# Optimization experiments

Hardware: AMD Instinct MI355X
Metric: run time of the kernel (lower is better)

## Reference

```python
import jax, jax.numpy as jnp
import numpy as np

NUM_CAPSULE = 32
DIM_CAPSULE = 16
ROUTINGS = 3
IN_CAPS = 144
IN_DIM = 8
EPS = 1e-7  # keras.backend.epsilon()


def setup_inputs() -> dict:
    key = jax.random.key(0)
    k1, k2 = jax.random.split(key)
    inputs = jax.random.normal(k1, (512, IN_CAPS, IN_DIM), dtype=jnp.float32)
    # glorot_uniform over shape [num_capsule, 144, dim_capsule, 8]
    fan_in, fan_out = IN_CAPS * IN_DIM, NUM_CAPSULE * DIM_CAPSULE
    limit = np.sqrt(6.0 / (fan_in + fan_out)).astype(np.float32)
    W = jax.random.uniform(k2, (NUM_CAPSULE, IN_CAPS, DIM_CAPSULE, IN_DIM),
                           minval=-limit, maxval=limit, dtype=jnp.float32)
    return {"inputs": inputs, "W": W}


def _squash(s):
    # s: [..., dim_capsule]
    n2 = jnp.sum(s * s, axis=-1, keepdims=True)
    return (n2 / (1.0 + n2)) * s / jnp.sqrt(n2 + EPS)


def reference(inputs, W):
    # inputs: [B, 144, 8]; W: [num_capsule, 144, dim_capsule, 8]
    # tile+einsum('abci,bcji->abcj') == broadcasted contraction over i
    inputs_hat = jnp.einsum('aci,bcji->abcj', inputs, W)  # [B, nc, 144, dc]
    b = jnp.zeros(inputs_hat.shape[:3], dtype=inputs_hat.dtype)  # [B, nc, 144]
    outputs = None
    for i in range(ROUTINGS):
        c = jax.nn.softmax(b, axis=1)                      # over num_capsule
        s = jnp.einsum('abc,abcd->abd', c, inputs_hat)     # [B, nc, dc]
        outputs = _squash(s)
        if i < ROUTINGS - 1:
            b = b + jnp.einsum('abd,abcd->abc', outputs, inputs_hat)
    return outputs
```

## Files before the change

kernel.cpp:

```cpp
#include <hip/hip_runtime.h>

#define NC 32
#define DC 16
#define INC 144
#define IND 8
#define NT 512
#define LG_S 152

#define HATL_OFF 0
#define HATH_OFF (NC * INC * IND + 8)
#define LG_OFF (HATH_OFF + NC * INC * IND)
#define OB_OFF (LG_OFF + NC * LG_S)
#define SMEM_HALVES (OB_OFF + NC * DC)
#define SMEM_BYTES (SMEM_HALVES * 2)

typedef _Float16 h2 __attribute__((ext_vector_type(2)));
typedef _Float16 h4v __attribute__((ext_vector_type(4)));
typedef _Float16 h8 __attribute__((ext_vector_type(8)));
typedef float f4 __attribute__((ext_vector_type(4)));

union H8 { h8 v; h2 p[4]; _Float16 e[8]; };
union WU { uint4 u; h8 v; h2 p[4]; };

#if __has_builtin(__builtin_amdgcn_fdot2)
__device__ __forceinline__ float fdot2(h2 a, h2 b, float c) {
    return __builtin_amdgcn_fdot2(a, b, c, false);
}
#else
__device__ __forceinline__ float fdot2(h2 a, h2 b, float c) {
    return c + (float)a[0] * (float)b[0] + (float)a[1] * (float)b[1];
}
#endif

__global__ void convw_kernel(const float* __restrict__ W, _Float16* __restrict__ Wh) {
    int i = blockIdx.x * 256 + threadIdx.x;
    int cg = i & 15, d = (i >> 4) & 15, bk = i >> 8;
    int k = bk % 9, b = bk / 9;
    const float* s = W + (((size_t)b * INC + cg + 16 * k) * DC + d) * IND;
    f4 v0 = *reinterpret_cast<const f4*>(s);
    f4 v1 = *reinterpret_cast<const f4*>(s + 4);
    H8 o;
    o.e[0] = (_Float16)v0[0]; o.e[1] = (_Float16)v0[1];
    o.e[2] = (_Float16)v0[2]; o.e[3] = (_Float16)v0[3];
    o.e[4] = (_Float16)v1[0]; o.e[5] = (_Float16)v1[1];
    o.e[6] = (_Float16)v1[2]; o.e[7] = (_Float16)v1[3];
    *reinterpret_cast<h8*>(Wh + (size_t)i * 8) = o.v;
}

#define R9(M)  M(0) M(1) M(2) M(3) M(4) M(5) M(6) M(7) M(8)
#define R16(M) M(0) M(1) M(2) M(3) M(4) M(5) M(6) M(7) M(8) M(9) M(10) M(11) M(12) M(13) M(14) M(15)

template <typename WT>
__global__ __launch_bounds__(NT)
__attribute__((amdgpu_waves_per_eu(2, 4)))
void caps_kernel(const float* __restrict__ xg, const WT* __restrict__ Wg,
                 float* __restrict__ out) {
    extern __shared__ __align__(16) _Float16 sm[];
    _Float16* lg = sm + LG_OFF;
    _Float16* o_buf = sm + OB_OFF;
    _Float16* x_h = lg;

    const int t = threadIdx.x;
    const int b = t >> 4;
    const int cg = t & 15;
    const int a = blockIdx.x;

    if (t < 288) {
        f4 v = reinterpret_cast<const f4*>(xg + (size_t)a * (INC * IND))[t];
        h4v hv;
        hv[0] = (_Float16)v[0]; hv[1] = (_Float16)v[1];
        hv[2] = (_Float16)v[2]; hv[3] = (_Float16)v[3];
        *reinterpret_cast<h4v*>(x_h + t * 4) = hv;
    }
    __syncthreads();

#define DECLS(D) float s##D;
    R16(DECLS)
#define ZEROS(D) s##D = 0.f;
    R16(ZEROS)

#define WADDR(K, DG) reinterpret_cast<const uint4*>( \
    reinterpret_cast<const char*>(Wg) + (size_t)(b * 9 + (K)) * 4096 + (DG) * 256 + cg * 16)

#define PREA(K) { wA0 = *WADDR(K,0); wA1 = *WADDR(K,1); wA2 = *WADDR(K,2); \
                  wA3 = *WADDR(K,3); wA4 = *WADDR(K,4); wA5 = *WADDR(K,5); \
                  wA6 = *WADDR(K,6); wA7 = *WADDR(K,7); }
#define PREB(K) { wB0 = *WADDR(K,8); wB1 = *WADDR(K,9); wB2 = *WADDR(K,10); \
                  wB3 = *WADDR(K,11); wB4 = *WADDR(K,12); wB5 = *WADDR(K,13); \
                  wB6 = *WADDR(K,14); wB7 = *WADDR(K,15); }

#define HD1R(WREG, T, E, SD) { \
    WU w; w.u = WREG; \
    float ac = fdot2(w.p[0], xv.p[0], 0.f); \
    ac = fdot2(w.p[1], xv.p[1], ac); \
    ac = fdot2(w.p[2], xv.p[2], ac); \
    ac = fdot2(w.p[3], xv.p[3], ac); \
    T.e[E] = (_Float16)ac; s##SD += ac; }

#define CMPA(T) HD1R(wA0,T,0,0) HD1R(wA1,T,1,1) HD1R(wA2,T,2,2) HD1R(wA3,T,3,3) \
                HD1R(wA4,T,4,4) HD1R(wA5,T,5,5) HD1R(wA6,T,6,6) HD1R(wA7,T,7,7)
#define CMPB(T) HD1R(wB0,T,0,8) HD1R(wB1,T,1,9) HD1R(wB2,T,2,10) HD1R(wB3,T,3,11) \
                HD1R(wB4,T,4,12) HD1R(wB5,T,5,13) HD1R(wB6,T,6,14) HD1R(wB7,T,7,15)

#define HPIPE(K, KN) { \
    const int c = cg + 16 * (K); \
    H8 xv; xv.v = *reinterpret_cast<const h8*>(x_h + c * IND); \
    H8 tL, tH; \
    CMPA(tL) \
    PREA(KN) \
    CMPB(tH) \
    PREB(KN) \
    *reinterpret_cast<h8*>(sm + HATL_OFF + (size_t)(b * INC + c) * 8) = tL.v; \
    *reinterpret_cast<h8*>(sm + HATH_OFF + (size_t)(b * INC + c) * 8) = tH.v; }

#define HD1F(T, E, DG) { \
    const float* wf = wfr + (DG) * IND; \
    f4 w0 = *reinterpret_cast<const f4*>(wf); \
    f4 w1 = *reinterpret_cast<const f4*>(wf + 4); \
    float ac = (float)xv.e[0] * w0[0]; \
    ac = fmaf((float)xv.e[1], w0[1], ac); \
    ac = fmaf((float)xv.e[2], w0[2], ac); \
    ac = fmaf((float)xv.e[3], w0[3], ac); \
    ac = fmaf((float)xv.e[4], w1[0], ac); \
    ac = fmaf((float)xv.e[5], w1[1], ac); \
    ac = fmaf((float)xv.e[6], w1[2], ac); \
    ac = fmaf((float)xv.e[7], w1[3], ac); \
    T.e[E] = (_Float16)ac; s##DG += ac; }

#define HSTEPF(K) { \
    const int c = cg + 16 * (K); \
    H8 xv; xv.v = *reinterpret_cast<const h8*>(x_h + c * IND); \
    const float* wfr = reinterpret_cast<const float*>(Wg) + \
                       (size_t)(b * INC + c) * (DC * IND); \
    H8 tL, tH; \
    HD1F(tL,0,0) HD1F(tL,1,1) HD1F(tL,2,2) HD1F(tL,3,3) \
    HD1F(tL,4,4) HD1F(tL,5,5) HD1F(tL,6,6) HD1F(tL,7,7) \
    HD1F(tH,0,8) HD1F(tH,1,9) HD1F(tH,2,10) HD1F(tH,3,11) \
    HD1F(tH,4,12) HD1F(tH,5,13) HD1F(tH,6,14) HD1F(tH,7,15) \
    *reinterpret_cast<h8*>(sm + HATL_OFF + (size_t)(b * INC + c) * 8) = tL.v; \
    *reinterpret_cast<h8*>(sm + HATH_OFF + (size_t)(b * INC + c) * 8) = tH.v; }

    if constexpr (sizeof(WT) == 2) {
        uint4 wA0, wA1, wA2, wA3, wA4, wA5, wA6, wA7;
        uint4 wB0, wB1, wB2, wB3, wB4, wB5, wB6, wB7;
        PREA(0) PREB(0)
        HPIPE(0, 1) HPIPE(1, 2) HPIPE(2, 3) HPIPE(3, 4) HPIPE(4, 5)
        HPIPE(5, 6) HPIPE(6, 7) HPIPE(7, 8) HPIPE(8, 8)
    } else {
        R9(HSTEPF)
    }
    __syncthreads();

    const bool c8 = (cg & 8) != 0, c4 = (cg & 4) != 0;
    const bool c2 = (cg & 2) != 0, c1 = (cg & 1) != 0;
#define HV(A, B, M, CB) { float snd_ = (CB) ? s##A : s##B; \
                          float kp_ = (CB) ? s##B : s##A; \
                          s##A = kp_ + __shfl_xor(snd_, M, 16); }
#define HALVE16 \
    HV(0,8,8,c8) HV(1,9,8,c8) HV(2,10,8,c8) HV(3,11,8,c8) \
    HV(4,12,8,c8) HV(5,13,8,c8) HV(6,14,8,c8) HV(7,15,8,c8) \
    HV(0,4,4,c4) HV(1,5,4,c4) HV(2,6,4,c4) HV(3,7,4,c4) \
    HV(0,2,2,c2) HV(1,3,2,c2) \
    HV(0,1,1,c1)

#define SQUASH1(RS, OVAL) \
    float r_ = s0 * (RS); \
    float n2_ = r_ * r_; \
    n2_ += __shfl_xor(n2_, 1, 16); n2_ += __shfl_xor(n2_, 2, 16); \
    n2_ += __shfl_xor(n2_, 4, 16); n2_ += __shfl_xor(n2_, 8, 16); \
    float OVAL = r_ * (n2_ / ((1.0f + n2_) * sqrtf(n2_ + 1e-7f)));

#define OBCAST(OVAL) \
    o_buf[b * DC + cg] = (_Float16)(OVAL); \
    __threadfence_block(); \
    oLv = *reinterpret_cast<const h8*>(o_buf + b * DC); \
    oHv = *reinterpret_cast<const h8*>(o_buf + b * DC + 8);

    h8 oLv, oHv;
    HALVE16
    {
        SQUASH1(1.0f / 32.0f, oval)
        OBCAST(oval)
    }

#define DECLG(K) float lgr##K = 0.f;
    R9(DECLG)

#define BSTEP(K) { \
    const int c = cg + 16 * (K); \
    H8 hl, hh; \
    hl.v = *reinterpret_cast<const h8*>(sm + HATL_OFF + (size_t)(b * INC + c) * 8); \
    hh.v = *reinterpret_cast<const h8*>(sm + HATH_OFF + (size_t)(b * INC + c) * 8); \
    H8 ol, oh; ol.v = oLv; oh.v = oHv; \
    float dt  = fdot2(hl.p[0], ol.p[0], 0.f); \
    float dt2 = fdot2(hl.p[1], ol.p[1], 0.f); \
    dt  = fdot2(hl.p[2], ol.p[2], dt); \
    dt2 = fdot2(hl.p[3], ol.p[3], dt2); \
    dt  = fdot2(hh.p[0], oh.p[0], dt); \
    dt2 = fdot2(hh.p[1], oh.p[1], dt2); \
    dt  = fdot2(hh.p[2], oh.p[2], dt); \
    dt2 = fdot2(hh.p[3], oh.p[3], dt2); \
    lgr##K += dt + dt2; \
    lg[b * LG_S + c] = (_Float16)lgr##K; }

#define SSTEP(K) { \
    const int c = cg + 16 * (K); \
    float cf = (float)lg[b * LG_S + c]; \
    H8 hl, hh; \
    hl.v = *reinterpret_cast<const h8*>(sm + HATL_OFF + (size_t)(b * INC + c) * 8); \
    hh.v = *reinterpret_cast<const h8*>(sm + HATH_OFF + (size_t)(b * INC + c) * 8); \
    s0  = fmaf(cf, (float)hl.e[0], s0);  s1  = fmaf(cf, (float)hl.e[1], s1); \
    s2  = fmaf(cf, (float)hl.e[2], s2);  s3  = fmaf(cf, (float)hl.e[3], s3); \
    s4  = fmaf(cf, (float)hl.e[4], s4);  s5  = fmaf(cf, (float)hl.e[5], s5); \
    s6  = fmaf(cf, (float)hl.e[6], s6);  s7  = fmaf(cf, (float)hl.e[7], s7); \
    s8  = fmaf(cf, (float)hh.e[0], s8);  s9  = fmaf(cf, (float)hh.e[1], s9); \
    s10 = fmaf(cf, (float)hh.e[2], s10); s11 = fmaf(cf, (float)hh.e[3], s11); \
    s12 = fmaf(cf, (float)hh.e[4], s12); s13 = fmaf(cf, (float)hh.e[5], s13); \
    s14 = fmaf(cf, (float)hh.e[6], s14); s15 = fmaf(cf, (float)hh.e[7], s15); }

    for (int it = 0; it < 2; ++it) {
        R9(BSTEP)
        __syncthreads();

        if (t < 2 * INC) {
            const int c = t >> 1;
            const int rb = (t & 1) * 16;
#define SMR(I) float v##I = (float)lg[(rb + I) * LG_S + c];
            R16(SMR)
            float m = fmaxf(v0, v1);
#define SMM(I) m = fmaxf(m, v##I);
            SMM(2) SMM(3) SMM(4) SMM(5) SMM(6) SMM(7) SMM(8) SMM(9)
            SMM(10) SMM(11) SMM(12) SMM(13) SMM(14) SMM(15)
            m = fmaxf(m, __shfl_xor(m, 1));
            float S = 0.f;
#define SME(I) v##I = __expf(v##I - m); S += v##I;
            R16(SME)
            S += __shfl_xor(S, 1);
            float inv = 1.0f / S;
#define SMW(I) lg[(rb + I) * LG_S + c] = (_Float16)(v##I * inv);
            R16(SMW)
        }
        __syncthreads();

        R16(ZEROS)
        R9(SSTEP)
        HALVE16

        if (it == 0) {
            SQUASH1(1.0f, oval)
            OBCAST(oval)
            __syncthreads();
        } else {
            SQUASH1(1.0f, oval)
            out[(size_t)a * (NC * DC) + t] = oval;
        }
    }
}

extern "C" void kernel_launch(void* const* d_in, const int* in_sizes, int n_in,
                              void* d_out, int out_size, void* d_ws, size_t ws_size,
                              hipStream_t stream) {
    const float* x = (const float*)d_in[0];
    const float* W = (const float*)d_in[1];
    float* out = (float*)d_out;

    const size_t WH_BYTES = (size_t)NC * INC * DC * IND * 2;

    if (ws_size >= WH_BYTES) {
        _Float16* Wh = (_Float16*)d_ws;
        hipLaunchKernelGGL(convw_kernel, dim3(288), dim3(256), 0, stream, W, Wh);
        hipFuncSetAttribute(reinterpret_cast<const void*>(&caps_kernel<_Float16>),
                            hipFuncAttributeMaxDynamicSharedMemorySize, SMEM_BYTES);
        hipLaunchKernelGGL(caps_kernel<_Float16>, dim3(512), dim3(NT), SMEM_BYTES,
                           stream, x, Wh, out);
    } else {
        hipFuncSetAttribute(reinterpret_cast<const void*>(&caps_kernel<float>),
                            hipFuncAttributeMaxDynamicSharedMemorySize, SMEM_BYTES);
        hipLaunchKernelGGL(caps_kernel<float>, dim3(512), dim3(NT), SMEM_BYTES,
                           stream, x, W, out);
    }
}
```

Measured before the change: 44.72 us.

## Split hat computation into separate kernel writing fp16 u_hat to global workspace

Adds a hat_kernel that caches one capsule's fp16 weights in LDS and computes inputs_hat for 16 batch rows per block, writing the results to global memory. A route_kernel then loads u_hat into LDS and runs routing only, with the first iteration's sum done by a plain reduction. The goal is to stop each routing block from streaming all weights out of global or L2 memory. In exchange it writes and rereads about 75 MB of u_hat through HBM and adds an extra launch. It needs a larger workspace, and the old fused path is kept as a fallback.

Measured after the change: 86.93 us. 94.4% more time.

```diff
diff --git a/kernel.cpp b/kernel.cpp
--- a/kernel.cpp
+++ b/kernel.cpp
@@ -13,6 +13,12 @@
 #define OB_OFF (LG_OFF + NC * LG_S)
 #define SMEM_HALVES (OB_OFF + NC * DC)
 #define SMEM_BYTES (SMEM_HALVES * 2)
+
+#define WH_BYTES ((size_t)NC * INC * DC * IND * 2)
+#define PLANE_HALVES ((size_t)512 * NC * INC * IND)
+#define PLANE_BYTES (PLANE_HALVES * 2)
+#define NEED_BYTES (WH_BYTES + 2 * PLANE_BYTES)
+#define HSM_BYTES 73728
 
 typedef _Float16 h2 __attribute__((ext_vector_type(2)));
 typedef _Float16 h4v __attribute__((ext_vector_type(4)));
@@ -47,30 +53,89 @@
     *reinterpret_cast<h8*>(Wh + (size_t)i * 8) = o.v;
 }
 
+#define R8(M)  M(0) M(1) M(2) M(3) M(4) M(5) M(6) M(7)
 #define R9(M)  M(0) M(1) M(2) M(3) M(4) M(5) M(6) M(7) M(8)
 #define R16(M) M(0) M(1) M(2) M(3) M(4) M(5) M(6) M(7) M(8) M(9) M(10) M(11) M(12) M(13) M(14) M(15)
 
-template <typename WT>
+__global__ __launch_bounds__(256)
+void hat_kernel(const float* __restrict__ xg, const _Float16* __restrict__ Wh,
+                _Float16* __restrict__ hatLg, _Float16* __restrict__ hatHg) {
+    extern __shared__ __align__(16) _Float16 hsm[];
+    _Float16* Wl = hsm;
+    _Float16* xl = hsm + 18432;
+
+    const int t = threadIdx.x;
+    const int b = blockIdx.x & 31;
+    const int ach = blockIdx.x >> 5;
+
+    {
+        const h8* src = reinterpret_cast<const h8*>(Wh + (size_t)b * 18432);
+        h8* dst = reinterpret_cast<h8*>(Wl);
+        #pragma unroll
+        for (int j = 0; j < 9; ++j) dst[t + 256 * j] = src[t + 256 * j];
+    }
+    {
+        const f4* src = reinterpret_cast<const f4*>(xg) + (size_t)ach * 4608;
+        #pragma unroll
+        for (int j = 0; j < 18; ++j) {
+            int i = t + 256 * j;
+            f4 v = src[i];
+            h4v hv;
+            hv[0] = (_Float16)v[0]; hv[1] = (_Float16)v[1];
+            hv[2] = (_Float16)v[2]; hv[3] = (_Float16)v[3];
+            *reinterpret_cast<h4v*>(xl + (size_t)i * 4) = hv;
+        }
+    }
+    __syncthreads();
+
+    const int al = t >> 4, cg = t & 15;
+    const size_t rowbase = (((size_t)(ach * 16 + al) * NC + b) * INC + cg * 9) * 8;
+
+#define WD1(T, E, D) { \
+    WU w; w.u = *reinterpret_cast<const uint4*>(Wl + ((kk * 16 + (D)) * 16 + cg) * 8); \
+    float ac = fdot2(w.p[0], xv.p[0], 0.f); \
+    ac = fdot2(w.p[1], xv.p[1], ac); \
+    ac = fdot2(w.p[2], xv.p[2], ac); \
+    ac = fdot2(w.p[3], xv.p[3], ac); \
+    T.e[E] = (_Float16)ac; }
+
+#define HK(K) { \
+    const int kk = (K); \
+    const int c = cg + 16 * kk; \
+    H8 xv; xv.v = *reinterpret_cast<const h8*>(xl + ((size_t)al * INC + c) * 8); \
+    H8 tL, tH; \
+    WD1(tL,0,0) WD1(tL,1,1) WD1(tL,2,2) WD1(tL,3,3) \
+    WD1(tL,4,4) WD1(tL,5,5) WD1(tL,6,6) WD1(tL,7,7) \
+    WD1(tH,0,8) WD1(tH,1,9) WD1(tH,2,10) WD1(tH,3,11) \
+    WD1(tH,4,12) WD1(tH,5,13) WD1(tH,6,14) WD1(tH,7,15) \
+    *reinterpret_cast<h8*>(hatLg + rowbase + (size_t)kk * 8) = tL.v; \
+    *reinterpret_cast<h8*>(hatHg + rowbase + (size_t)kk * 8) = tH.v; }
+
+    R9(HK)
+}
+
 __global__ __launch_bounds__(NT)
 __attribute__((amdgpu_waves_per_eu(2, 4)))
-void caps_kernel(const float* __restrict__ xg, const WT* __restrict__ Wg,
-                 float* __restrict__ out) {
+void route_kernel(const _Float16* __restrict__ hatLg, const _Float16* __restrict__ hatHg,
+                  float* __restrict__ out) {
     extern __shared__ __align__(16) _Float16 sm[];
     _Float16* lg = sm + LG_OFF;
     _Float16* o_buf = sm + OB_OFF;
-    _Float16* x_h = lg;
 
     const int t = threadIdx.x;
     const int b = t >> 4;
     const int cg = t & 15;
     const int a = blockIdx.x;
 
-    if (t < 288) {
-        f4 v = reinterpret_cast<const f4*>(xg + (size_t)a * (INC * IND))[t];
-        h4v hv;
-        hv[0] = (_Float16)v[0]; hv[1] = (_Float16)v[1];
-        hv[2] = (_Float16)v[2]; hv[3] = (_Float16)v[3];
-        *reinterpret_cast<h4v*>(x_h + t * 4) = hv;
+    {
+        const h8* srcL = reinterpret_cast<const h8*>(hatLg + (size_t)a * 36864);
+        const h8* srcH = reinterpret_cast<const h8*>(hatHg + (size_t)a * 36864);
+        #pragma unroll
+        for (int j = 0; j < 9; ++j) {
+            int i = t + NT * j;
+            *reinterpret_cast<h8*>(sm + HATL_OFF + (size_t)i * 8) = srcL[i];
+            *reinterpret_cast<h8*>(sm + HATH_OFF + (size_t)i * 8) = srcH[i];
+        }
     }
     __syncthreads();
 
@@ -79,77 +144,21 @@
 #define ZEROS(D) s##D = 0.f;
     R16(ZEROS)
 
-#define WADDR(K, DG) reinterpret_cast<const uint4*>( \
-    reinterpret_cast<const char*>(Wg) + (size_t)(b * 9 + (K)) * 4096 + (DG) * 256 + cg * 16)
-
-#define PREA(K) { wA0 = *WADDR(K,0); wA1 = *WADDR(K,1); wA2 = *WADDR(K,2); \
-                  wA3 = *WADDR(K,3); wA4 = *WADDR(K,4); wA5 = *WADDR(K,5); \
-                  wA6 = *WADDR(K,6); wA7 = *WADDR(K,7); }
-#define PREB(K) { wB0 = *WADDR(K,8); wB1 = *WADDR(K,9); wB2 = *WADDR(K,10); \
-                  wB3 = *WADDR(K,11); wB4 = *WADDR(K,12); wB5 = *WADDR(K,13); \
-                  wB6 = *WADDR(K,14); wB7 = *WADDR(K,15); }
-
-#define HD1R(WREG, T, E, SD) { \
-    WU w; w.u = WREG; \
-    float ac = fdot2(w.p[0], xv.p[0], 0.f); \
-    ac = fdot2(w.p[1], xv.p[1], ac); \
-    ac = fdot2(w.p[2], xv.p[2], ac); \
-    ac = fdot2(w.p[3], xv.p[3], ac); \
-    T.e[E] = (_Float16)ac; s##SD += ac; }
-
-#define CMPA(T) HD1R(wA0,T,0,0) HD1R(wA1,T,1,1) HD1R(wA2,T,2,2) HD1R(wA3,T,3,3) \
-                HD1R(wA4,T,4,4) HD1R(wA5,T,5,5) HD1R(wA6,T,6,6) HD1R(wA7,T,7,7)
-#define CMPB(T) HD1R(wB0,T,0,8) HD1R(wB1,T,1,9) HD1R(wB2,T,2,10) HD1R(wB3,T,3,11) \
-                HD1R(wB4,T,4,12) HD1R(wB5,T,5,13) HD1R(wB6,T,6,14) HD1R(wB7,T,7,15)
-
-#define HPIPE(K, KN) { \
-    const int c = cg + 16 * (K); \
-    H8 xv; xv.v = *reinterpret_cast<const h8*>(x_h + c * IND); \
-    H8 tL, tH; \
-    CMPA(tL) \
-    PREA(KN) \
-    CMPB(tH) \
-    PREB(KN) \
-    *reinterpret_cast<h8*>(sm + HATL_OFF + (size_t)(b * INC + c) * 8) = tL.v; \
-    *reinterpret_cast<h8*>(sm + HATH_OFF + (size_t)(b * INC + c) * 8) = tH.v; }
-
-#define HD1F(T, E, DG) { \
-    const float* wf = wfr + (DG) * IND; \
-    f4 w0 = *reinterpret_cast<const f4*>(wf); \
-    f4 w1 = *reinterpret_cast<const f4*>(wf + 4); \
-    float ac = (float)xv.e[0] * w0[0]; \
-    ac = fmaf((float)xv.e[1], w0[1], ac); \
-    ac = fmaf((float)xv.e[2], w0[2], ac); \
-    ac = fmaf((float)xv.e[3], w0[3], ac); \
-    ac = fmaf((float)xv.e[4], w1[0], ac); \
-    ac = fmaf((float)xv.e[5], w1[1], ac); \
-    ac = fmaf((float)xv.e[6], w1[2], ac); \
-    ac = fmaf((float)xv.e[7], w1[3], ac); \
-    T.e[E] = (_Float16)ac; s##DG += ac; }
-
-#define HSTEPF(K) { \
-    const int c = cg + 16 * (K); \
-    H8 xv; xv.v = *reinterpret_cast<const h8*>(x_h + c * IND); \
-    const float* wfr = reinterpret_cast<const float*>(Wg) + \
-                       (size_t)(b * INC + c) * (DC * IND); \
-    H8 tL, tH; \
-    HD1F(tL,0,0) HD1F(tL,1,1) HD1F(tL,2,2) HD1F(tL,3,3) \
-    HD1F(tL,4,4) HD1F(tL,5,5) HD1F(tL,6,6) HD1F(tL,7,7) \
-    HD1F(tH,0,8) HD1F(tH,1,9) HD1F(tH,2,10) HD1F(tH,3,11) \
-    HD1F(tH,4,12) HD1F(tH,5,13) HD1F(tH,6,14) HD1F(tH,7,15) \
-    *reinterpret_cast<h8*>(sm + HATL_OFF + (size_t)(b * INC + c) * 8) = tL.v; \
-    *reinterpret_cast<h8*>(sm + HATH_OFF + (size_t)(b * INC + c) * 8) = tH.v; }
-
-    if constexpr (sizeof(WT) == 2) {
-        uint4 wA0, wA1, wA2, wA3, wA4, wA5, wA6, wA7;
-        uint4 wB0, wB1, wB2, wB3, wB4, wB5, wB6, wB7;
-        PREA(0) PREB(0)
-        HPIPE(0, 1) HPIPE(1, 2) HPIPE(2, 3) HPIPE(3, 4) HPIPE(4, 5)
-        HPIPE(5, 6) HPIPE(6, 7) HPIPE(7, 8) HPIPE(8, 8)
-    } else {
-        R9(HSTEPF)
-    }
-    __syncthreads();
+#define S0STEP(K) { \
+    const size_t r_ = ((size_t)b * INC + cg * 9 + (K)) * 8; \
+    H8 hl, hh; \
+    hl.v = *reinterpret_cast<const h8*>(sm + HATL_OFF + r_); \
+    hh.v = *reinterpret_cast<const h8*>(sm + HATH_OFF + r_); \
+    s0  += (float)hl.e[0];  s1  += (float)hl.e[1]; \
+    s2  += (float)hl.e[2];  s3  += (float)hl.e[3]; \
+    s4  += (float)hl.e[4];  s5  += (float)hl.e[5]; \
+    s6  += (float)hl.e[6];  s7  += (float)hl.e[7]; \
+    s8  += (float)hh.e[0];  s9  += (float)hh.e[1]; \
+    s10 += (float)hh.e[2];  s11 += (float)hh.e[3]; \
+    s12 += (float)hh.e[4];  s13 += (float)hh.e[5]; \
+    s14 += (float)hh.e[6];  s15 += (float)hh.e[7]; }
+
+    R9(S0STEP)
 
     const bool c8 = (cg & 8) != 0, c4 = (cg & 4) != 0;
     const bool c2 = (cg & 2) != 0, c1 = (cg & 1) != 0;
@@ -186,11 +195,12 @@
 #define DECLG(K) float lgr##K = 0.f;
     R9(DECLG)
 
-#define BSTEP(K) { \
+#define RBSTEP(K) { \
+    const size_t r_ = ((size_t)b * INC + cg * 9 + (K)) * 8; \
     const int c = cg + 16 * (K); \
     H8 hl, hh; \
-    hl.v = *reinterpret_cast<const h8*>(sm + HATL_OFF + (size_t)(b * INC + c) * 8); \
-    hh.v = *reinterpret_cast<const h8*>(sm + HATH_OFF + (size_t)(b * INC + c) * 8); \
+    hl.v = *reinterpret_cast<const h8*>(sm + HATL_OFF + r_); \
+    hh.v = *reinterpret_cast<const h8*>(sm + HATH_OFF + r_); \
     H8 ol, oh; ol.v = oLv; oh.v = oHv; \
     float dt  = fdot2(hl.p[0], ol.p[0], 0.f); \
     float dt2 = fdot2(hl.p[1], ol.p[1], 0.f); \
@@ -203,12 +213,13 @@
     lgr##K += dt + dt2; \
     lg[b * LG_S + c] = (_Float16)lgr##K; }
 
-#define SSTEP(K) { \
+#define RSSTEP(K) { \
+    const size_t r_ = ((size_t)b * INC + cg * 9 + (K)) * 8; \
     const int c = cg + 16 * (K); \
     float cf = (float)lg[b * LG_S + c]; \
     H8 hl, hh; \
-    hl.v = *reinterpret_cast<const h8*>(sm + HATL_OFF + (size_t)(b * INC + c) * 8); \
-    hh.v = *reinterpret_cast<const h8*>(sm + HATH_OFF + (size_t)(b * INC + c) * 8); \
+    hl.v = *reinterpret_cast<const h8*>(sm + HATL_OFF + r_); \
+    hh.v = *reinterpret_cast<const h8*>(sm + HATH_OFF + r_); \
     s0  = fmaf(cf, (float)hl.e[0], s0);  s1  = fmaf(cf, (float)hl.e[1], s1); \
     s2  = fmaf(cf, (float)hl.e[2], s2);  s3  = fmaf(cf, (float)hl.e[3], s3); \
     s4  = fmaf(cf, (float)hl.e[4], s4);  s5  = fmaf(cf, (float)hl.e[5], s5); \
@@ -219,7 +230,7 @@
     s14 = fmaf(cf, (float)hh.e[6], s14); s15 = fmaf(cf, (float)hh.e[7], s15); }
 
     for (int it = 0; it < 2; ++it) {
-        R9(BSTEP)
+        R9(RBSTEP)
         __syncthreads();
 
         if (t < 2 * INC) {
@@ -243,7 +254,7 @@
         __syncthreads();
 
         R16(ZEROS)
-        R9(SSTEP)
+        R9(RSSTEP)
         HALVE16
 
         if (it == 0) {
@@ -257,6 +268,184 @@
     }
 }
 
+template <typename WT>
+__global__ __launch_bounds__(NT)
+__attribute__((amdgpu_waves_per_eu(2, 4)))
+void caps_kernel(const float* __restrict__ xg, const WT* __restrict__ Wg,
+                 float* __restrict__ out) {
+    extern __shared__ __align__(16) _Float16 sm[];
+    _Float16* lg = sm + LG_OFF;
+    _Float16* o_buf = sm + OB_OFF;
+    _Float16* x_h = lg;
+
+    const int t = threadIdx.x;
+    const int b = t >> 4;
+    const int cg = t & 15;
+    const int a = blockIdx.x;
+
+    if (t < 288) {
+        f4 v = reinterpret_cast<const f4*>(xg + (size_t)a * (INC * IND))[t];
+        h4v hv;
+        hv[0] = (_Float16)v[0]; hv[1] = (_Float16)v[1];
+        hv[2] = (_Float16)v[2]; hv[3] = (_Float16)v[3];
+        *reinterpret_cast<h4v*>(x_h + t * 4) = hv;
+    }
+    __syncthreads();
+
+    R16(DECLS)
+    R16(ZEROS)
+
+#define WADDR(K, DG) reinterpret_cast<const uint4*>( \
+    reinterpret_cast<const char*>(Wg) + (size_t)(b * 9 + (K)) * 4096 + (DG) * 256 + cg * 16)
+
+#define PREA(K) { wA0 = *WADDR(K,0); wA1 = *WADDR(K,1); wA2 = *WADDR(K,2); \
+                  wA3 = *WADDR(K,3); wA4 = *WADDR(K,4); wA5 = *WADDR(K,5); \
+                  wA6 = *WADDR(K,6); wA7 = *WADDR(K,7); }
+#define PREB(K) { wB0 = *WADDR(K,8); wB1 = *WADDR(K,9); wB2 = *WADDR(K,10); \
+                  wB3 = *WADDR(K,11); wB4 = *WADDR(K,12); wB5 = *WADDR(K,13); \
+                  wB6 = *WADDR(K,14); wB7 = *WADDR(K,15); }
+
+#define HD1R(WREG, T, E, SD) { \
+    WU w; w.u = WREG; \
+    float ac = fdot2(w.p[0], xv.p[0], 0.f); \
+    ac = fdot2(w.p[1], xv.p[1], ac); \
+    ac = fdot2(w.p[2], xv.p[2], ac); \
+    ac = fdot2(w.p[3], xv.p[3], ac); \
+    T.e[E] = (_Float16)ac; s##SD += ac; }
+
+#define CMPA(T) HD1R(wA0,T,0,0) HD1R(wA1,T,1,1) HD1R(wA2,T,2,2) HD1R(wA3,T,3,3) \
+                HD1R(wA4,T,4,4) HD1R(wA5,T,5,5) HD1R(wA6,T,6,6) HD1R(wA7,T,7,7)
+#define CMPB(T) HD1R(wB0,T,0,8) HD1R(wB1,T,1,9) HD1R(wB2,T,2,10) HD1R(wB3,T,3,11) \
+                HD1R(wB4,T,4,12) HD1R(wB5,T,5,13) HD1R(wB6,T,6,14) HD1R(wB7,T,7,15)
+
+#define HPIPE(K, KN) { \
+    const int c = cg + 16 * (K); \
+    H8 xv; xv.v = *reinterpret_cast<const h8*>(x_h + c * IND); \
+    H8 tL, tH; \
+    CMPA(tL) \
+    PREA(KN) \
+    CMPB(tH) \
+    PREB(KN) \
+    *reinterpret_cast<h8*>(sm + HATL_OFF + (size_t)(b * INC + c) * 8) = tL.v; \
+    *reinterpret_cast<h8*>(sm + HATH_OFF + (size_t)(b * INC + c) * 8) = tH.v; }
+
+#define HD1F(T, E, DG) { \
+    const float* wf = wfr + (DG) * IND; \
+    f4 w0 = *reinterpret_cast<const f4*>(wf); \
+    f4 w1 = *reinterpret_cast<const f4*>(wf + 4); \
+    float ac = (float)xv.e[0] * w0[0]; \
+    ac = fmaf((float)xv.e[1], w0[1], ac); \
+    ac = fmaf((float)xv.e[2], w0[2], ac); \
+    ac = fmaf((float)xv.e[3], w0[3], ac); \
+    ac = fmaf((float)xv.e[4], w1[0], ac); \
+    ac = fmaf((float)xv.e[5], w1[1], ac); \
+    ac = fmaf((float)xv.e[6], w1[2], ac); \
+    ac = fmaf((float)xv.e[7], w1[3], ac); \
+    T.e[E] = (_Float16)ac; s##DG += ac; }
+
+#define HSTEPF(K) { \
+    const int c = cg + 16 * (K); \
+    H8 xv; xv.v = *reinterpret_cast<const h8*>(x_h + c * IND); \
+    const float* wfr = reinterpret_cast<const float*>(Wg) + \
+                       (size_t)(b * INC + c) * (DC * IND); \
+    H8 tL, tH; \
+    HD1F(tL,0,0) HD1F(tL,1,1) HD1F(tL,2,2) HD1F(tL,3,3) \
+    HD1F(tL,4,4) HD1F(tL,5,5) HD1F(tL,6,6) HD1F(tL,7,7) \
+    HD1F(tH,0,8) HD1F(tH,1,9) HD1F(tH,2,10) HD1F(tH,3,11) \
+    HD1F(tH,4,12) HD1F(tH,5,13) HD1F(tH,6,14) HD1F(tH,7,15) \
+    *reinterpret_cast<h8*>(sm + HATL_OFF + (size_t)(b * INC + c) * 8) = tL.v; \
+    *reinterpret_cast<h8*>(sm + HATH_OFF + (size_t)(b * INC + c) * 8) = tH.v; }
+
+    if constexpr (sizeof(WT) == 2) {
+        uint4 wA0, wA1, wA2, wA3, wA4, wA5, wA6, wA7;
+        uint4 wB0, wB1, wB2, wB3, wB4, wB5, wB6, wB7;
+        PREA(0) PREB(0)
+        HPIPE(0, 1) HPIPE(1, 2) HPIPE(2, 3) HPIPE(3, 4) HPIPE(4, 5)
+        HPIPE(5, 6) HPIPE(6, 7) HPIPE(7, 8) HPIPE(8, 8)
+    } else {
+        R9(HSTEPF)
+    }
+    __syncthreads();
+
+    const bool c8 = (cg & 8) != 0, c4 = (cg & 4) != 0;
+    const bool c2 = (cg & 2) != 0, c1 = (cg & 1) != 0;
+
+    h8 oLv, oHv;
+    HALVE16
+    {
+        SQUASH1(1.0f / 32.0f, oval)
+        OBCAST(oval)
+    }
+
+    R9(DECLG)
+
+#define BSTEP(K) { \
+    const int c = cg + 16 * (K); \
+    H8 hl, hh; \
+    hl.v = *reinterpret_cast<const h8*>(sm + HATL_OFF + (size_t)(b * INC + c) * 8); \
+    hh.v = *reinterpret_cast<const h8*>(sm + HATH_OFF + (size_t)(b * INC + c) * 8); \
+    H8 ol, oh; ol.v = oLv; oh.v = oHv; \
+    float dt  = fdot2(hl.p[0], ol.p[0], 0.f); \
+    float dt2 = fdot2(hl.p[1], ol.p[1], 0.f); \
+    dt  = fdot2(hl.p[2], ol.p[2], dt); \
+    dt2 = fdot2(hl.p[3], ol.p[3], dt2); \
+    dt  = fdot2(hh.p[0], oh.p[0], dt); \
+    dt2 = fdot2(hh.p[1], oh.p[1], dt2); \
+    dt  = fdot2(hh.p[2], oh.p[2], dt); \
+    dt2 = fdot2(hh.p[3], oh.p[3], dt2); \
+    lgr##K += dt + dt2; \
+    lg[b * LG_S + c] = (_Float16)lgr##K; }
+
+#define SSTEP(K) { \
+    const int c = cg + 16 * (K); \
+    float cf = (float)lg[b * LG_S + c]; \
+    H8 hl, hh; \
+    hl.v = *reinterpret_cast<const h8*>(sm + HATL_OFF + (size_t)(b * INC + c) * 8); \
+    hh.v = *reinterpret_cast<const h8*>(sm + HATH_OFF + (size_t)(b * INC + c) * 8); \
+    s0  = fmaf(cf, (float)hl.e[0], s0);  s1  = fmaf(cf, (float)hl.e[1], s1); \
+    s2  = fmaf(cf, (float)hl.e[2], s2);  s3  = fmaf(cf, (float)hl.e[3], s3); \
+    s4  = fmaf(cf, (float)hl.e[4], s4);  s5  = fmaf(cf, (float)hl.e[5], s5); \
+    s6  = fmaf(cf, (float)hl.e[6], s6);  s7  = fmaf(cf, (float)hl.e[7], s7); \
+    s8  = fmaf(cf, (float)hh.e[0], s8);  s9  = fmaf(cf, (float)hh.e[1], s9); \
+    s10 = fmaf(cf, (float)hh.e[2], s10); s11 = fmaf(cf, (float)hh.e[3], s11); \
+    s12 = fmaf(cf, (float)hh.e[4], s12); s13 = fmaf(cf, (float)hh.e[5], s13); \
+    s14 = fmaf(cf, (float)hh.e[6], s14); s15 = fmaf(cf, (float)hh.e[7], s15); }
+
+    for (int it = 0; it < 2; ++it) {
+        R9(BSTEP)
+        __syncthreads();
+
+        if (t < 2 * INC) {
+            const int c = t >> 1;
+            const int rb = (t & 1) * 16;
+            R16(SMR)
+            float m = fmaxf(v0, v1);
+            SMM(2) SMM(3) SMM(4) SMM(5) SMM(6) SMM(7) SMM(8) SMM(9)
+            SMM(10) SMM(11) SMM(12) SMM(13) SMM(14) SMM(15)
+            m = fmaxf(m, __shfl_xor(m, 1));
+            float S = 0.f;
+            R16(SME)
+            S += __shfl_xor(S, 1);
+            float inv = 1.0f / S;
+            R16(SMW)
+        }
+        __syncthreads();
+
+        R16(ZEROS)
+        R9(SSTEP)
+        HALVE16
+
+        if (it == 0) {
+            SQUASH1(1.0f, oval)
+            OBCAST(oval)
+            __syncthreads();
+        } else {
+            SQUASH1(1.0f, oval)
+            out[(size_t)a * (NC * DC) + t] = oval;
+        }
+    }
+}
+
 extern "C" void kernel_launch(void* const* d_in, const int* in_sizes, int n_in,
                               void* d_out, int out_size, void* d_ws, size_t ws_size,
                               hipStream_t stream) {
@@ -264,9 +453,20 @@
     const float* W = (const float*)d_in[1];
     float* out = (float*)d_out;
 
-    const size_t WH_BYTES = (size_t)NC * INC * DC * IND * 2;
-
-    if (ws_size >= WH_BYTES) {
+    if (ws_size >= NEED_BYTES) {
+        _Float16* Wh = (_Float16*)d_ws;
+        _Float16* hatLg = (_Float16*)((char*)d_ws + WH_BYTES);
+        _Float16* hatHg = (_Float16*)((char*)d_ws + WH_BYTES + PLANE_BYTES);
+        hipLaunchKernelGGL(convw_kernel, dim3(288), dim3(256), 0, stream, W, Wh);
+        hipFuncSetAttribute(reinterpret_cast<const void*>(&hat_kernel),
+                            hipFuncAttributeMaxDynamicSharedMemorySize, HSM_BYTES);
+        hipLaunchKernelGGL(hat_kernel, dim3(1024), dim3(256), HSM_BYTES, stream,
+                           x, Wh, hatLg, hatHg);
+        hipFuncSetAttribute(reinterpret_cast<const void*>(&route_kernel),
+                            hipFuncAttributeMaxDynamicSharedMemorySize, SMEM_BYTES);
+        hipLaunchKernelGGL(route_kernel, dim3(512), dim3(NT), SMEM_BYTES, stream,
+                           hatLg, hatHg, out);
+    } else if (ws_size >= WH_BYTES) {
         _Float16* Wh = (_Float16*)d_ws;
         hipLaunchKernelGGL(convw_kernel, dim3(288), dim3(256), 0, stream, W, Wh);
         hipFuncSetAttribute(reinterpret_cast<const void*>(&caps_kernel<_Float16>),
```

## Keep inputs_hat in registers instead of shared memory

Applied to the files above, without the earlier changes.

Stores each thread's per-capsule prediction vectors in registers across the routing iterations rather than writing them to and rereading them from LDS, and shrinks shared memory to small static arrays. This removes the LDS traffic in the routing loops and a barrier, and lowers LDS use so more blocks can be resident. The explicit W prefetch pipeline and waves-per-EU hint are dropped, so register pressure and load-latency hiding now depend on the compiler, with spill risk.

Result: slower. 51.20 us (+14.5%).

```diff
diff --git a/kernel.cpp b/kernel.cpp
--- a/kernel.cpp
+++ b/kernel.cpp
@@ -6,13 +6,6 @@
 #define IND 8
 #define NT 512
 #define LG_S 152
-
-#define HATL_OFF 0
-#define HATH_OFF (NC * INC * IND + 8)
-#define LG_OFF (HATH_OFF + NC * INC * IND)
-#define OB_OFF (LG_OFF + NC * LG_S)
-#define SMEM_HALVES (OB_OFF + NC * DC)
-#define SMEM_BYTES (SMEM_HALVES * 2)
 
 typedef _Float16 h2 __attribute__((ext_vector_type(2)));
 typedef _Float16 h4v __attribute__((ext_vector_type(4)));
@@ -52,13 +45,11 @@
 
 template <typename WT>
 __global__ __launch_bounds__(NT)
-__attribute__((amdgpu_waves_per_eu(2, 4)))
 void caps_kernel(const float* __restrict__ xg, const WT* __restrict__ Wg,
                  float* __restrict__ out) {
-    extern __shared__ __align__(16) _Float16 sm[];
-    _Float16* lg = sm + LG_OFF;
-    _Float16* o_buf = sm + OB_OFF;
-    _Float16* x_h = lg;
+    __shared__ __align__(16) _Float16 x_h[INC * IND];
+    __shared__ __align__(16) _Float16 lg[NC * LG_S];
+    __shared__ __align__(16) _Float16 o_buf[NC * DC];
 
     const int t = threadIdx.x;
     const int b = t >> 4;
@@ -74,44 +65,20 @@
     }
     __syncthreads();
 
+#define DECLH(K) uint4 hL##K, hH##K;
+    R9(DECLH)
 #define DECLS(D) float s##D;
     R16(DECLS)
 #define ZEROS(D) s##D = 0.f;
     R16(ZEROS)
 
-#define WADDR(K, DG) reinterpret_cast<const uint4*>( \
-    reinterpret_cast<const char*>(Wg) + (size_t)(b * 9 + (K)) * 4096 + (DG) * 256 + cg * 16)
-
-#define PREA(K) { wA0 = *WADDR(K,0); wA1 = *WADDR(K,1); wA2 = *WADDR(K,2); \
-                  wA3 = *WADDR(K,3); wA4 = *WADDR(K,4); wA5 = *WADDR(K,5); \
-                  wA6 = *WADDR(K,6); wA7 = *WADDR(K,7); }
-#define PREB(K) { wB0 = *WADDR(K,8); wB1 = *WADDR(K,9); wB2 = *WADDR(K,10); \
-                  wB3 = *WADDR(K,11); wB4 = *WADDR(K,12); wB5 = *WADDR(K,13); \
-                  wB6 = *WADDR(K,14); wB7 = *WADDR(K,15); }
-
-#define HD1R(WREG, T, E, SD) { \
-    WU w; w.u = WREG; \
+#define HD1(T, E, DG) { \
+    WU w; w.u = *reinterpret_cast<const uint4*>(wrb + (DG) * 256); \
     float ac = fdot2(w.p[0], xv.p[0], 0.f); \
     ac = fdot2(w.p[1], xv.p[1], ac); \
     ac = fdot2(w.p[2], xv.p[2], ac); \
     ac = fdot2(w.p[3], xv.p[3], ac); \
-    T.e[E] = (_Float16)ac; s##SD += ac; }
-
-#define CMPA(T) HD1R(wA0,T,0,0) HD1R(wA1,T,1,1) HD1R(wA2,T,2,2) HD1R(wA3,T,3,3) \
-                HD1R(wA4,T,4,4) HD1R(wA5,T,5,5) HD1R(wA6,T,6,6) HD1R(wA7,T,7,7)
-#define CMPB(T) HD1R(wB0,T,0,8) HD1R(wB1,T,1,9) HD1R(wB2,T,2,10) HD1R(wB3,T,3,11) \
-                HD1R(wB4,T,4,12) HD1R(wB5,T,5,13) HD1R(wB6,T,6,14) HD1R(wB7,T,7,15)
-
-#define HPIPE(K, KN) { \
-    const int c = cg + 16 * (K); \
-    H8 xv; xv.v = *reinterpret_cast<const h8*>(x_h + c * IND); \
-    H8 tL, tH; \
-    CMPA(tL) \
-    PREA(KN) \
-    CMPB(tH) \
-    PREB(KN) \
-    *reinterpret_cast<h8*>(sm + HATL_OFF + (size_t)(b * INC + c) * 8) = tL.v; \
-    *reinterpret_cast<h8*>(sm + HATH_OFF + (size_t)(b * INC + c) * 8) = tH.v; }
+    T.e[E] = (_Float16)ac; s##DG += ac; }
 
 #define HD1F(T, E, DG) { \
     const float* wf = wfr + (DG) * IND; \
@@ -127,29 +94,29 @@
     ac = fmaf((float)xv.e[7], w1[3], ac); \
     T.e[E] = (_Float16)ac; s##DG += ac; }
 
-#define HSTEPF(K) { \
+#define HSTEP(K) { \
     const int c = cg + 16 * (K); \
     H8 xv; xv.v = *reinterpret_cast<const h8*>(x_h + c * IND); \
-    const float* wfr = reinterpret_cast<const float*>(Wg) + \
-                       (size_t)(b * INC + c) * (DC * IND); \
     H8 tL, tH; \
-    HD1F(tL,0,0) HD1F(tL,1,1) HD1F(tL,2,2) HD1F(tL,3,3) \
-    HD1F(tL,4,4) HD1F(tL,5,5) HD1F(tL,6,6) HD1F(tL,7,7) \
-    HD1F(tH,0,8) HD1F(tH,1,9) HD1F(tH,2,10) HD1F(tH,3,11) \
-    HD1F(tH,4,12) HD1F(tH,5,13) HD1F(tH,6,14) HD1F(tH,7,15) \
-    *reinterpret_cast<h8*>(sm + HATL_OFF + (size_t)(b * INC + c) * 8) = tL.v; \
-    *reinterpret_cast<h8*>(sm + HATH_OFF + (size_t)(b * INC + c) * 8) = tH.v; }
-
-    if constexpr (sizeof(WT) == 2) {
-        uint4 wA0, wA1, wA2, wA3, wA4, wA5, wA6, wA7;
-        uint4 wB0, wB1, wB2, wB3, wB4, wB5, wB6, wB7;
-        PREA(0) PREB(0)
-        HPIPE(0, 1) HPIPE(1, 2) HPIPE(2, 3) HPIPE(3, 4) HPIPE(4, 5)
-        HPIPE(5, 6) HPIPE(6, 7) HPIPE(7, 8) HPIPE(8, 8)
-    } else {
-        R9(HSTEPF)
-    }
-    __syncthreads();
+    if constexpr (sizeof(WT) == 2) { \
+        const char* wrb = reinterpret_cast<const char*>(Wg) + \
+                          (size_t)(b * 9 + (K)) * 4096 + cg * 16; \
+        HD1(tL,0,0) HD1(tL,1,1) HD1(tL,2,2) HD1(tL,3,3) \
+        HD1(tL,4,4) HD1(tL,5,5) HD1(tL,6,6) HD1(tL,7,7) \
+        HD1(tH,0,8) HD1(tH,1,9) HD1(tH,2,10) HD1(tH,3,11) \
+        HD1(tH,4,12) HD1(tH,5,13) HD1(tH,6,14) HD1(tH,7,15) \
+    } else { \
+        const float* wfr = reinterpret_cast<const float*>(Wg) + \
+                           (size_t)(b * INC + c) * (DC * IND); \
+        HD1F(tL,0,0) HD1F(tL,1,1) HD1F(tL,2,2) HD1F(tL,3,3) \
+        HD1F(tL,4,4) HD1F(tL,5,5) HD1F(tL,6,6) HD1F(tL,7,7) \
+        HD1F(tH,0,8) HD1F(tH,1,9) HD1F(tH,2,10) HD1F(tH,3,11) \
+        HD1F(tH,4,12) HD1F(tH,5,13) HD1F(tH,6,14) HD1F(tH,7,15) \
+    } \
+    WU uL, uH; uL.v = tL.v; uH.v = tH.v; \
+    hL##K = uL.u; hH##K = uH.u; }
+
+    R9(HSTEP)
 
     const bool c8 = (cg & 8) != 0, c4 = (cg & 4) != 0;
     const bool c2 = (cg & 2) != 0, c1 = (cg & 1) != 0;
@@ -187,10 +154,7 @@
     R9(DECLG)
 
 #define BSTEP(K) { \
-    const int c = cg + 16 * (K); \
-    H8 hl, hh; \
-    hl.v = *reinterpret_cast<const h8*>(sm + HATL_OFF + (size_t)(b * INC + c) * 8); \
-    hh.v = *reinterpret_cast<const h8*>(sm + HATH_OFF + (size_t)(b * INC + c) * 8); \
+    WU hl, hh; hl.u = hL##K; hh.u = hH##K; \
     H8 ol, oh; ol.v = oLv; oh.v = oHv; \
     float dt  = fdot2(hl.p[0], ol.p[0], 0.f); \
     float dt2 = fdot2(hl.p[1], ol.p[1], 0.f); \
@@ -201,22 +165,20 @@
     dt  = fdot2(hh.p[2], oh.p[2], dt); \
     dt2 = fdot2(hh.p[3], oh.p[3], dt2); \
     lgr##K += dt + dt2; \
-    lg[b * LG_S + c] = (_Float16)lgr##K; }
+    lg[b * LG_S + cg + 16 * (K)] = (_Float16)lgr##K; }
 
 #define SSTEP(K) { \
-    const int c = cg + 16 * (K); \
-    float cf = (float)lg[b * LG_S + c]; \
-    H8 hl, hh; \
-    hl.v = *reinterpret_cast<const h8*>(sm + HATL_OFF + (size_t)(b * INC + c) * 8); \
-    hh.v = *reinterpret_cast<const h8*>(sm + HATH_OFF + (size_t)(b * INC + c) * 8); \
-    s0  = fmaf(cf, (float)hl.e[0], s0);  s1  = fmaf(cf, (float)hl.e[1], s1); \
-    s2  = fmaf(cf, (float)hl.e[2], s2);  s3  = fmaf(cf, (float)hl.e[3], s3); \
-    s4  = fmaf(cf, (float)hl.e[4], s4);  s5  = fmaf(cf, (float)hl.e[5], s5); \
-    s6  = fmaf(cf, (float)hl.e[6], s6);  s7  = fmaf(cf, (float)hl.e[7], s7); \
-    s8  = fmaf(cf, (float)hh.e[0], s8);  s9  = fmaf(cf, (float)hh.e[1], s9); \
-    s10 = fmaf(cf, (float)hh.e[2], s10); s11 = fmaf(cf, (float)hh.e[3], s11); \
-    s12 = fmaf(cf, (float)hh.e[4], s12); s13 = fmaf(cf, (float)hh.e[5], s13); \
-    s14 = fmaf(cf, (float)hh.e[6], s14); s15 = fmaf(cf, (float)hh.e[7], s15); }
+    float cf = (float)lg[b * LG_S + cg + 16 * (K)]; \
+    WU hl, hh; hl.u = hL##K; hh.u = hH##K; \
+    H8 hle, hhe; hle.v = hl.v; hhe.v = hh.v; \
+    s0  = fmaf(cf, (float)hle.e[0], s0);  s1  = fmaf(cf, (float)hle.e[1], s1); \
+    s2  = fmaf(cf, (float)hle.e[2], s2);  s3  = fmaf(cf, (float)hle.e[3], s3); \
+    s4  = fmaf(cf, (float)hle.e[4], s4);  s5  = fmaf(cf, (float)hle.e[5], s5); \
+    s6  = fmaf(cf, (float)hle.e[6], s6);  s7  = fmaf(cf, (float)hle.e[7], s7); \
+    s8  = fmaf(cf, (float)hhe.e[0], s8);  s9  = fmaf(cf, (float)hhe.e[1], s9); \
+    s10 = fmaf(cf, (float)hhe.e[2], s10); s11 = fmaf(cf, (float)hhe.e[3], s11); \
+    s12 = fmaf(cf, (float)hhe.e[4], s12); s13 = fmaf(cf, (float)hhe.e[5], s13); \
+    s14 = fmaf(cf, (float)hhe.e[6], s14); s15 = fmaf(cf, (float)hhe.e[7], s15); }
 
     for (int it = 0; it < 2; ++it) {
         R9(BSTEP)
@@ -269,14 +231,10 @@
     if (ws_size >= WH_BYTES) {
         _Float16* Wh = (_Float16*)d_ws;
         hipLaunchKernelGGL(convw_kernel, dim3(288), dim3(256), 0, stream, W, Wh);
-        hipFuncSetAttribute(reinterpret_cast<const void*>(&caps_kernel<_Float16>),
-                            hipFuncAttributeMaxDynamicSharedMemorySize, SMEM_BYTES);
-        hipLaunchKernelGGL(caps_kernel<_Float16>, dim3(512), dim3(NT), SMEM_BYTES,
+        hipLaunchKernelGGL(caps_kernel<_Float16>, dim3(512), dim3(NT), 0,
                            stream, x, Wh, out);
     } else {
-        hipFuncSetAttribute(reinterpret_cast<const void*>(&caps_kernel<float>),
-                            hipFuncAttributeMaxDynamicSharedMemorySize, SMEM_BYTES);
-        hipLaunchKernelGGL(caps_kernel<float>, dim3(512), dim3(NT), SMEM_BYTES,
+        hipLaunchKernelGGL(caps_kernel<float>, dim3(512), dim3(NT), 0,
                            stream, x, W, out);
     }
 }
```
